# Kernel optimization log

Hardware: AMD Instinct MI355X
Metric: run time of the kernel (lower is better)

The kernel has to match this reference:

```python
import jax, jax.numpy as jnp
import numpy as np

B, S, D, H, L, FFN = 32, 512, 512, 8, 4, 1024
DH = D // H
EPS = 1e-5


def make_pe(seq, d):
    pos = np.arange(seq)[:, None].astype(np.float64)
    i = np.arange(d)[None, :]
    angle = pos / np.power(10000.0, (i // 2 * 2.0) / d)
    pe = angle.copy()
    pe[:, 0::2] = np.sin(angle[:, 0::2])
    pe[:, 1::2] = np.cos(angle[:, 1::2])
    return jnp.asarray(pe, dtype=jnp.float32)


def layer_norm(x, g, b):
    mu = jnp.mean(x, axis=-1, keepdims=True)
    var = jnp.mean((x - mu) ** 2, axis=-1, keepdims=True)
    return (x - mu) * jax.lax.rsqrt(var + EPS) * g + b


def setup_inputs() -> dict:
    key = jax.random.key(0)
    ks = jax.random.split(key, 12)
    sd = 0.02
    d = {
        "x": jax.random.normal(ks[0], (B, S, D), dtype=jnp.float32),
        "pe": make_pe(S, D),
        "Wq": jax.random.normal(ks[1], (L, D, D), dtype=jnp.float32) * sd,
        "bq": jnp.zeros((L, D), dtype=jnp.float32),
        "Wk": jax.random.normal(ks[2], (L, D, D), dtype=jnp.float32) * sd,
        "bk": jnp.zeros((L, D), dtype=jnp.float32),
        "Wv": jax.random.normal(ks[3], (L, D, D), dtype=jnp.float32) * sd,
        "bv": jnp.zeros((L, D), dtype=jnp.float32),
        "Wo": jax.random.normal(ks[4], (L, D, D), dtype=jnp.float32) * sd,
        "bo": jnp.zeros((L, D), dtype=jnp.float32),
        "ln1_g": jnp.ones((L, D), dtype=jnp.float32),
        "ln1_b": jnp.zeros((L, D), dtype=jnp.float32),
        "W1": jax.random.normal(ks[5], (L, D, FFN), dtype=jnp.float32) * sd,
        "b1": jnp.zeros((L, FFN), dtype=jnp.float32),
        "W2": jax.random.normal(ks[6], (L, FFN, D), dtype=jnp.float32) * sd,
        "b2": jnp.zeros((L, D), dtype=jnp.float32),
        "ln2_g": jnp.ones((L, D), dtype=jnp.float32),
        "ln2_b": jnp.zeros((L, D), dtype=jnp.float32),
    }
    return d


def reference(x, pe, Wq, bq, Wk, bk, Wv, bv, Wo, bo, ln1_g, ln1_b,
              W1, b1, W2, b2, ln2_g, ln2_b):
    out = x + pe  # positional encoding (dropout = identity in eval)
    scale = DH ** (-0.5)
    for l in range(L):
        # projections (B,S,D)
        Q = out @ Wq[l] + bq[l]
        K = out @ Wk[l] + bk[l]
        V = out @ Wv[l] + bv[l]
        # faithful raw view (no head transpose), matching torch .view semantics
        Qh = Q.reshape(B * H, S, DH)
        Kh = K.reshape(B * H, S, DH)
        Vh = V.reshape(B * H, S, DH)
        att = jnp.einsum('bqd,bkd->bqk', Qh, Kh) * scale  # (B*H,S,S)
        att = jax.nn.softmax(att, axis=-1)
        ctx = jnp.einsum('bqk,bkd->bqd', att, Vh).reshape(B, S, D)
        a = layer_norm(ctx @ Wo[l] + bo[l] + out, ln1_g[l], ln1_b[l])
        # position-wise FFN
        h = jax.nn.relu(a @ W1[l] + b1[l])
        out = layer_norm(h @ W2[l] + b2[l] + a, ln2_g[l], ln2_b[l])
    return out.reshape(B, S * D)
```

## Files before the change

### kernel.cpp

```cpp
#include <hip/hip_runtime.h>
#include <stdint.h>

#define NB 32
#define NS 512
#define ND 512
#define NH 8
#define NL 4
#define NF 1024
#define NDH 64
#define NM (NB*NS)
#define WLSTRIDE 2097152
#define CSCALE 0.18033688f

typedef __attribute__((ext_vector_type(8))) short bf16x8;
typedef __attribute__((ext_vector_type(4))) short s16x4;
typedef __attribute__((ext_vector_type(4))) float f32x4;
typedef __attribute__((ext_vector_type(2))) uint32_t u32x2;

#define VM0  asm volatile("s_waitcnt vmcnt(0)" ::: "memory")
#define VM4  asm volatile("s_waitcnt vmcnt(4)" ::: "memory")
#define VM8  asm volatile("s_waitcnt vmcnt(8)" ::: "memory")
#define SCHB __builtin_amdgcn_sched_barrier(0)
#define SB   __builtin_amdgcn_s_barrier()

__device__ __forceinline__ short f2bf(float f) {
    union { float f; uint32_t u; } v; v.f = f;
    uint32_t r = (v.u + 0x7FFFu + ((v.u >> 16) & 1u)) >> 16;
    return (short)r;
}
__device__ __forceinline__ float bf2f(short s) {
    union { uint32_t u; float f; } v; v.u = ((uint32_t)(uint16_t)s) << 16;
    return v.f;
}
__device__ __forceinline__ f32x4 mfma16(bf16x8 a, bf16x8 b, f32x4 c) {
    return __builtin_amdgcn_mfma_f32_16x16x32_bf16(a, b, c, 0, 0, 0);
}
__device__ __forceinline__ void gld16(const void* g, void* l) {
    __builtin_amdgcn_global_load_lds(
        (const __attribute__((address_space(1))) void*)g,
        (__attribute__((address_space(3))) void*)l, 16, 0, 0);
}
__device__ __forceinline__ uint32_t cvtpk(float a, float b) {
    uint32_t w;
    asm("v_cvt_pk_bf16_f32 %0, %1, %2" : "=v"(w) : "v"(a), "v"(b));
    return w;
}
__device__ __forceinline__ void xcd_swz(int& bx, int& by, int gx, int gy) {
    int n = gx * gy;
    int f = by * gx + bx;
    int q = n >> 3;
    int xcd = f & 7, idx = f >> 3;
    int s = xcd * q + idx;
    bx = s % gx; by = s / gx;
}

__global__ __launch_bounds__(256) void convT_k(const float* __restrict__ src,
        short* __restrict__ dst, int K, int N, int woff)
{
    __shared__ float T[64][65];
    int tk = K >> 6, tn = N >> 6;
    int bid = blockIdx.x;
    int l = bid / (tk * tn), rb = bid % (tk * tn);
    int k0 = (rb / tn) << 6, n0 = (rb % tn) << 6;
    const float* s = src + (size_t)l * K * N;
    short* d = dst + (size_t)l * WLSTRIDE + woff;
    int tr = threadIdx.x >> 4, tc = threadIdx.x & 15;
    #pragma unroll
    for (int p = 0; p < 4; p++) {
        int row = p * 16 + tr;
        f32x4 v = *(const f32x4*)(s + (size_t)(k0 + row) * N + n0 + tc * 4);
        #pragma unroll
        for (int j = 0; j < 4; j++) T[row][tc * 4 + j] = v[j];
    }
    __syncthreads();
    #pragma unroll
    for (int p = 0; p < 4; p++) {
        int nrow = p * 16 + tr;
        s16x4 w;
        #pragma unroll
        for (int j = 0; j < 4; j++) w[j] = f2bf(T[tc * 4 + j][nrow]);
        *(s16x4*)(d + (size_t)(n0 + nrow) * K + k0 + tc * 4) = w;
    }
}

__global__ __launch_bounds__(256) void biaspack_k(const float* __restrict__ bq,
        const float* __restrict__ bk, const float* __restrict__ bv, float* __restrict__ out)
{
    int i = blockIdx.x * 256 + threadIdx.x;
    if (i >= NL * 1536) return;
    int l = i / 1536, j = i - l * 1536;
    float v = (j < 512) ? bq[l * 512 + j] * CSCALE
            : (j < 1024) ? bk[l * 512 + j - 512] : bv[l * 512 + j - 1024];
    out[i] = v;
}

__global__ __launch_bounds__(256) void addpe_k(const float* __restrict__ x,
        const float* __restrict__ pe, short* __restrict__ X)
{
    size_t i = ((size_t)blockIdx.x * 256 + threadIdx.x) * 8;
    size_t sd = i % (size_t)(NS * ND);
    f32x4 a0 = *(const f32x4*)(x + i);
    f32x4 a1 = *(const f32x4*)(x + i + 4);
    f32x4 p0 = *(const f32x4*)(pe + sd);
    f32x4 p1 = *(const f32x4*)(pe + sd + 4);
    bf16x8 r;
    #pragma unroll
    for (int j = 0; j < 4; j++) { r[j] = f2bf(a0[j] + p0[j]); r[4 + j] = f2bf(a1[j] + p1[j]); }
    *(bf16x8*)(X + i) = r;
}

template<int EPI>
__global__ __launch_bounds__(256) void gemm_bt(
        const short* __restrict__ A, const short* __restrict__ Bt,
        const float* __restrict__ bias, const short* __restrict__ res,
        void* __restrict__ C0, void* __restrict__ C1, void* __restrict__ C2,
        int M, int N, int K)
{
    __shared__ __align__(16) short Al[16384];
    __shared__ __align__(16) short Bl[16384];
    const int tid = threadIdx.x;
    const int wid = tid >> 6, lane = tid & 63;
    int bx = blockIdx.x, by = blockIdx.y;
    xcd_swz(bx, by, gridDim.x, gridDim.y);
    const int m0 = by * 128, n0 = bx * 128;
    const int wr = wid >> 1, wc = wid & 1;

    f32x4 acc[4][4];
    f32x4 zz = {0.f, 0.f, 0.f, 0.f};
    #pragma unroll
    for (int i = 0; i < 4; i++)
        #pragma unroll
        for (int j = 0; j < 4; j++) acc[i][j] = zz;

    const size_t rk = (size_t)K * 2;
    const char* Ab = (const char*)A + (size_t)m0 * rk;
    const char* Bb = (const char*)Bt + (size_t)n0 * rk;

    int srA[4], scA[4], srB[4], scB[4];
    #pragma unroll
    for (int c = 0; c < 4; c++) {
        int p = c * 4096 + tid * 16;
        int la = p ^ (((p >> 7) & 7) << 4);
        srA[c] = la >> 7;  scA[c] = la & 127;
        int lb = p ^ (((p >> 9) & 7) << 4);
        srB[c] = lb >> 7;  scB[c] = lb & 127;
    }

    auto stage = [&](int dofs, int kt) {
        size_t kb = (size_t)(kt << 6) * 2;
        #pragma unroll
        for (int c = 0; c < 4; c++)
            gld16(Ab + (size_t)srA[c] * rk + kb + scA[c],
                  (char*)Al + dofs + c * 4096 + wid * 1024);
        #pragma unroll
        for (int c = 0; c < 4; c++)
            gld16(Bb + (size_t)srB[c] * rk + kb + scB[c],
                  (char*)Bl + dofs + c * 4096 + wid * 1024);
    };
    auto compute = [&](int dofs) {
        #pragma unroll
        for (int ks = 0; ks < 2; ks++) {
            bf16x8 af[4], bfr[4];
            #pragma unroll
            for (int mf = 0; mf < 4; mf++) {
                int row = wr * 64 + mf * 16 + (lane & 15);
                int off = (row * 128 + ks * 64 + ((lane >> 4) * 16)) ^ ((row & 7) << 4);
                af[mf] = *(const bf16x8*)((const char*)Al + dofs + off);
            }
            #pragma unroll
            for (int nf = 0; nf < 4; nf++) {
                int row = wc * 64 + ((lane & 15) << 2) + nf;
                int off = row * 128
                        + ((ks * 64 + ((lane >> 4) * 16)) ^ (((row >> 2) & 7) << 4));
                bfr[nf] = *(const bf16x8*)((const char*)Bl + dofs + off);
            }
            #pragma unroll
            for (int mf = 0; mf < 4; mf++)
                #pragma unroll
                for (int nf = 0; nf < 4; nf++)
                    acc[mf][nf] = mfma16(af[mf], bfr[nf], acc[mf][nf]);
        }
    };

    const int nt = K >> 6;
    stage(0, 0);
    stage(16384, 1);
    VM8; SCHB; SB;
    for (int t = 0; t < nt; t += 2) {
        compute(0);
        SB;
        if (t + 2 < nt) { stage(0, t + 2); VM8; } else VM0;
        SCHB; SB;
        compute(16384);
        SB;
        if (t + 3 < nt) { stage(16384, t + 3); VM8; } else VM0;
        SCHB; SB;
    }

    int seg = 0;
    void* outp;
    int colbase, ostride;
    if (EPI == 0) {
        seg = n0 >> 9;
        outp = (seg == 0) ? C0 : (seg == 1) ? C1 : C2;
        colbase = n0 & 511; ostride = 512;
    } else {
        outp = C0; colbase = n0; ostride = N;
    }

    const int c0 = wc * 64 + ((lane & 15) << 2);
    f32x4 bi4 = *(const f32x4*)(bias + n0 + c0);
    #pragma unroll
    for (int mf = 0; mf < 4; mf++) {
        #pragma unroll
        for (int r = 0; r < 4; r++) {
            int row = m0 + wr * 64 + mf * 16 + ((lane >> 4) << 2) + r;
            float v[4];
            #pragma unroll
            for (int j = 0; j < 4; j++) {
                if (EPI == 0 && seg == 0) v[j] = fmaf(acc[mf][j][r], CSCALE, bi4[j]);
                else                      v[j] = acc[mf][j][r] + bi4[j];
            }
            if (EPI == 0) {
                u32x2 w; w[0] = cvtpk(v[0], v[1]); w[1] = cvtpk(v[2], v[3]);
                *(u32x2*)((short*)outp + (size_t)row * 512 + colbase + c0) = w;
            } else if (EPI == 1) {
                u32x2 w;
                w[0] = cvtpk(fmaxf(v[0], 0.f), fmaxf(v[1], 0.f));
                w[1] = cvtpk(fmaxf(v[2], 0.f), fmaxf(v[3], 0.f));
                *(u32x2*)((short*)outp + (size_t)row * ostride + colbase + c0) = w;
            } else {
                s16x4 rr = *(const s16x4*)(res + (size_t)row * ostride + colbase + c0);
                f32x4 o4;
                #pragma unroll
                for (int j = 0; j < 4; j++) o4[j] = v[j] + bf2f(rr[j]);
                *(f32x4*)((float*)outp + (size_t)row * ostride + colbase + c0) = o4;
            }
        }
    }
}

__global__ __launch_bounds__(256) void vtrans_k(const short* __restrict__ V,
        short* __restrict__ VT)
{
    __shared__ short T[64][65];
    const int tid = threadIdx.x;
    const int r0 = blockIdx.x * 64, g = blockIdx.y;
    const size_t base = (size_t)g * 32768;
    #pragma unroll
    for (int rep = 0; rep < 2; rep++) {
        int chunk = rep * 256 + tid;
        int sr = chunk >> 3, c8 = (chunk & 7) * 8;
        bf16x8 v = *(const bf16x8*)(V + base + (size_t)(r0 + sr) * 64 + c8);
        #pragma unroll
        for (int j = 0; j < 8; j++) T[sr][c8 + j] = v[j];
    }
    __syncthreads();
    #pragma unroll
    for (int rep = 0; rep < 2; rep++) {
        int chunk = rep * 256 + tid;
        int dh = chunk >> 3, c8 = (chunk & 7) * 8;
        bf16x8 w;
        #pragma unroll
        for (int j = 0; j < 8; j++) w[j] = T[c8 + j][dh];
        *(bf16x8*)(VT + base + (size_t)dh * 512 + r0 + c8) = w;
    }
}

__global__ __launch_bounds__(256) void attn_k(
        const short* __restrict__ Q, const short* __restrict__ Kb,
        const short* __restrict__ VT, short* __restrict__ ctx)
{
    __shared__ __align__(16) short Kl[8192];
    __shared__ __align__(16) short Vl[8192];
    __shared__ __align__(16) short Pl[8192];
    const int tid = threadIdx.x, wid = tid >> 6, lane = tid & 63;
    int bx = blockIdx.x, by = blockIdx.y;
    xcd_swz(bx, by, gridDim.x, gridDim.y);
    const int g = by, q0 = bx * 128;
    const size_t base = (size_t)g * 32768;

    bf16x8 qa[2][2];
    #pragma unroll
    for (int qf = 0; qf < 2; qf++)
        #pragma unroll
        for (int ks = 0; ks < 2; ks++)
            qa[qf][ks] = *(const bf16x8*)(Q + base
                + (size_t)(q0 + wid * 32 + qf * 16 + (lane & 15)) * 64
                + ks * 32 + ((lane >> 4) * 8));

    f32x4 o[2][4];
    float ps[2][4];
    f32x4 zz = {0.f, 0.f, 0.f, 0.f};
    #pragma unroll
    for (int qf = 0; qf < 2; qf++) {
        #pragma unroll
        for (int nf = 0; nf < 4; nf++) o[qf][nf] = zz;
        #pragma unroll
        for (int r = 0; r < 4; r++) ps[qf][r] = 0.f;
    }

    const char* Kbase = (const char*)(Kb + base);
    const char* Vbase = (const char*)(VT + base);

    int ksp[2], srow[2], scol[2];
    #pragma unroll
    for (int c = 0; c < 2; c++) {
        int p = c * 4096 + tid * 16;
        ksp[c] = p ^ (((p >> 9) & 7) << 4);
        srow[c] = ksp[c] >> 7;  scol[c] = ksp[c] & 127;
    }

    auto stage = [&](int dofs, int kt) {
        #pragma unroll
        for (int c = 0; c < 2; c++)
            gld16(Kbase + (size_t)kt * 8192 + ksp[c],
                  (char*)Kl + dofs + c * 4096 + wid * 1024);
        #pragma unroll
        for (int c = 0; c < 2; c++)
            gld16(Vbase + (size_t)srow[c] * 1024 + kt * 128 + scol[c],
                  (char*)Vl + dofs + c * 4096 + wid * 1024);
    };

    auto tile = [&](int dofs) {
        f32x4 sc[2][4];
        #pragma unroll
        for (int qf = 0; qf < 2; qf++)
            #pragma unroll
            for (int nf = 0; nf < 4; nf++) sc[qf][nf] = zz;
        #pragma unroll
        for (int ks = 0; ks < 2; ks++) {
            #pragma unroll
            for (int nf = 0; nf < 4; nf++) {
                int kvr = ((lane & 15) << 2) + nf;
                int bo = kvr * 128
                       + ((ks * 64 + ((lane >> 4) * 16)) ^ (((kvr >> 2) & 7) << 4)) + dofs;
                bf16x8 kf = *(const bf16x8*)((const char*)Kl + bo);
                #pragma unroll
                for (int qf = 0; qf < 2; qf++)
                    sc[qf][nf] = mfma16(qa[qf][ks], kf, sc[qf][nf]);
            }
        }

        #pragma unroll
        for (int qf = 0; qf < 2; qf++) {
            #pragma unroll
            for (int r = 0; r < 4; r++) {
                int qr = wid * 32 + qf * 16 + ((lane >> 4) << 2) + r;
                float e0 = __builtin_amdgcn_exp2f(sc[qf][0][r]);
                float e1 = __builtin_amdgcn_exp2f(sc[qf][1][r]);
                float e2 = __builtin_amdgcn_exp2f(sc[qf][2][r]);
                float e3 = __builtin_amdgcn_exp2f(sc[qf][3][r]);
                ps[qf][r] += (e0 + e1) + (e2 + e3);
                u32x2 w;
                w[0] = cvtpk(e0, e1);
                w[1] = cvtpk(e2, e3);
                int bo = (qr * 128 + (lane & 15) * 8) ^ ((qr & 7) << 4);
                *(u32x2*)((char*)Pl + bo) = w;
            }
        }

        #pragma unroll
        for (int ks = 0; ks < 2; ks++) {
            bf16x8 pa[2];
            #pragma unroll
            for (int qf = 0; qf < 2; qf++) {
                int qrb = wid * 32 + qf * 16 + (lane & 15);
                int bo = (qrb * 128 + ks * 64 + ((lane >> 4) * 16)) ^ ((qrb & 7) << 4);
                pa[qf] = *(const bf16x8*)((const char*)Pl + bo);
            }
            #pragma unroll
            for (int nf = 0; nf < 4; nf++) {
                int dh = ((lane & 15) << 2) + nf;
                int bo2 = dh * 128
                        + ((ks * 64 + ((lane >> 4) * 16)) ^ (((dh >> 2) & 7) << 4)) + dofs;
                bf16x8 vf = *(const bf16x8*)((const char*)Vl + bo2);
                #pragma unroll
                for (int qf = 0; qf < 2; qf++)
                    o[qf][nf] = mfma16(pa[qf], vf, o[qf][nf]);
            }
        }
    };

    stage(0, 0);
    stage(8192, 1);
    VM4; SCHB; SB;
    for (int kt = 0; kt < 8; kt += 2) {
        tile(0);
        SB;
        if (kt + 2 < 8) { stage(0, kt + 2); VM4; } else VM0;
        SCHB; SB;
        tile(8192);
        SB;
        if (kt + 3 < 8) { stage(8192, kt + 3); VM4; } else VM0;
        SCHB; SB;
    }

    #pragma unroll
    for (int qf = 0; qf < 2; qf++) {
        #pragma unroll
        for (int r = 0; r < 4; r++) {
            float s = ps[qf][r];
            s += __shfl_xor(s, 1);
            s += __shfl_xor(s, 2);
            s += __shfl_xor(s, 4);
            s += __shfl_xor(s, 8);
            float inv = 1.f / s;
            int qr = q0 + wid * 32 + qf * 16 + ((lane >> 4) << 2) + r;
            u32x2 w;
            w[0] = cvtpk(o[qf][0][r] * inv, o[qf][1][r] * inv);
            w[1] = cvtpk(o[qf][2][r] * inv, o[qf][3][r] * inv);
            *(u32x2*)(ctx + base + (size_t)qr * 64 + ((lane & 15) << 2)) = w;
        }
    }
}

template<int OUTF32>
__global__ __launch_bounds__(256) void ln_k(
        const float* __restrict__ pre, const float* __restrict__ g,
        const float* __restrict__ b, void* __restrict__ out)
{
    int row = blockIdx.x * 4 + (threadIdx.x >> 6);
    int lane = threadIdx.x & 63;
    const float* x = pre + (size_t)row * ND + lane * 8;
    f32x4 a0 = *(const f32x4*)x;
    f32x4 a1 = *(const f32x4*)(x + 4);
    float s = 0.f, sq = 0.f;
    #pragma unroll
    for (int j = 0; j < 4; j++) { s += a0[j]; sq += a0[j] * a0[j]; s += a1[j]; sq += a1[j] * a1[j]; }
    #pragma unroll
    for (int d = 1; d < 64; d <<= 1) { s += __shfl_xor(s, d); sq += __shfl_xor(sq, d); }
    float mean = s * (1.f / ND);
    float var = sq * (1.f / ND) - mean * mean;
    float rstd = rsqrtf(var + 1e-5f);
    const float* gp = g + lane * 8;
    const float* bp = b + lane * 8;
    if (OUTF32) {
        float* op = (float*)out + (size_t)row * ND + lane * 8;
        f32x4 r0, r1;
        #pragma unroll
        for (int j = 0; j < 4; j++) {
            r0[j] = (a0[j] - mean) * rstd * gp[j] + bp[j];
            r1[j] = (a1[j] - mean) * rstd * gp[4 + j] + bp[4 + j];
        }
        *(f32x4*)op = r0;
        *(f32x4*)(op + 4) = r1;
    } else {
        bf16x8 rr;
        #pragma unroll
        for (int j = 0; j < 4; j++) {
            rr[j]     = f2bf((a0[j] - mean) * rstd * gp[j] + bp[j]);
            rr[4 + j] = f2bf((a1[j] - mean) * rstd * gp[4 + j] + bp[4 + j]);
        }
        *(bf16x8*)((short*)out + (size_t)row * ND + lane * 8) = rr;
    }
}

extern "C" void kernel_launch(void* const* d_in, const int* in_sizes, int n_in,
                              void* d_out, int out_size, void* d_ws, size_t ws_size,
                              hipStream_t stream)
{
    (void)in_sizes; (void)n_in; (void)out_size; (void)ws_size;
    const float* x   = (const float*)d_in[0];
    const float* pe  = (const float*)d_in[1];
    const float* Wq  = (const float*)d_in[2];
    const float* bq  = (const float*)d_in[3];
    const float* Wk  = (const float*)d_in[4];
    const float* bk  = (const float*)d_in[5];
    const float* Wv  = (const float*)d_in[6];
    const float* bv  = (const float*)d_in[7];
    const float* Wo  = (const float*)d_in[8];
    const float* bo  = (const float*)d_in[9];
    const float* g1  = (const float*)d_in[10];
    const float* be1 = (const float*)d_in[11];
    const float* W1  = (const float*)d_in[12];
    const float* b1  = (const float*)d_in[13];
    const float* W2  = (const float*)d_in[14];
    const float* b2  = (const float*)d_in[15];
    const float* g2  = (const float*)d_in[16];
    const float* be2 = (const float*)d_in[17];

    char* ws = (char*)d_ws;
    const size_t MB = 1048576;
    short* WT   = (short*)(ws);
    short* XB   = (short*)(ws + 16 * MB);
    short* QB   = (short*)(ws + 32 * MB);
    short* KB   = (short*)(ws + 48 * MB);
    short* VB   = (short*)(ws + 64 * MB);
    short* VTb  = (short*)(ws + 80 * MB);
    short* CT   = (short*)(ws + 96 * MB);
    float* BQKV = (float*)(ws + 112 * MB);
    short* AB   = QB;
    float* PR   = (float*)KB;
    short* HB   = VTb;

    convT_k<<<dim3(NL*8*8),  256, 0, stream>>>(Wq, WT, ND, ND, 0);
    convT_k<<<dim3(NL*8*8),  256, 0, stream>>>(Wk, WT, ND, ND, 262144);
    convT_k<<<dim3(NL*8*8),  256, 0, stream>>>(Wv, WT, ND, ND, 524288);
    convT_k<<<dim3(NL*8*8),  256, 0, stream>>>(Wo, WT, ND, ND, 786432);
    convT_k<<<dim3(NL*8*16), 256, 0, stream>>>(W1, WT, ND, NF, 1048576);
    convT_k<<<dim3(NL*16*8), 256, 0, stream>>>(W2, WT, NF, ND, 1572864);
    biaspack_k<<<dim3(24), 256, 0, stream>>>(bq, bk, bv, BQKV);

    addpe_k<<<dim3(4096), 256, 0, stream>>>(x, pe, XB);

    for (int l = 0; l < NL; l++) {
        const short* wl = WT + (size_t)l * WLSTRIDE;
        gemm_bt<0><<<dim3(12, 128), 256, 0, stream>>>(XB, wl, BQKV + l*1536, nullptr,
                                                      QB, KB, VB, NM, 1536, ND);
        vtrans_k<<<dim3(8, 256), 256, 0, stream>>>(VB, VTb);
        attn_k<<<dim3(4, 256), 256, 0, stream>>>(QB, KB, VTb, CT);
        gemm_bt<2><<<dim3(4, 128), 256, 0, stream>>>(CT, wl + 786432, bo + l*ND, XB,
                                                     PR, nullptr, nullptr, NM, ND, ND);
        ln_k<0><<<dim3(4096), 256, 0, stream>>>(PR, g1 + l*ND, be1 + l*ND, AB);
        gemm_bt<1><<<dim3(8, 128), 256, 0, stream>>>(AB, wl + 1048576, b1 + l*NF, nullptr,
                                                     HB, nullptr, nullptr, NM, NF, ND);
        gemm_bt<2><<<dim3(4, 128), 256, 0, stream>>>(HB, wl + 1572864, b2 + l*ND, AB,
                                                     PR, nullptr, nullptr, NM, ND, NF);
        if (l < NL - 1)
            ln_k<0><<<dim3(4096), 256, 0, stream>>>(PR, g2 + l*ND, be2 + l*ND, XB);
        else
            ln_k<1><<<dim3(4096), 256, 0, stream>>>(PR, g2 + l*ND, be2 + l*ND, (float*)d_out);
    }
}
```

Baseline: 761.1 us.

## Use 256x256-tile 512-thread GEMM for QKV and FFN1 projections

Adds a gemm_big kernel with 256x256 output tiles, 8 waves and 64KB of LDS per stage pair. The QKV projection and the first FFN GEMM now use it, roughly doubling operand reuse per byte loaded from global memory. The residual-epilogue GEMM is specialised to EPI 2 only, and both kernels precompute per-chunk global pointers to cut address arithmetic. Larger tiles mean fewer blocks (384 and 256) and higher register and LDS pressure, which may lower occupancy and load balance across CUs.

Result: no change. 767.5 us (+0.8%).

```diff
diff --git a/kernel.cpp b/kernel.cpp
--- a/kernel.cpp
+++ b/kernel.cpp
@@ -110,11 +110,133 @@
 }
 
 template<int EPI>
+__global__ __launch_bounds__(512) void gemm_big(
+        const short* __restrict__ A, const short* __restrict__ Bt,
+        const float* __restrict__ bias,
+        void* __restrict__ C0, void* __restrict__ C1, void* __restrict__ C2,
+        int M, int N, int K)
+{
+    __shared__ __align__(16) short Al[32768];
+    __shared__ __align__(16) short Bl[32768];
+    const int tid = threadIdx.x;
+    const int wid = tid >> 6, lane = tid & 63;
+    int bx = blockIdx.x, by = blockIdx.y;
+    xcd_swz(bx, by, gridDim.x, gridDim.y);
+    const int m0 = by * 256, n0 = bx * 256;
+    const int wr = wid >> 2, wc = wid & 3;
+
+    f32x4 acc[8][4];
+    f32x4 zz = {0.f, 0.f, 0.f, 0.f};
+    #pragma unroll
+    for (int i = 0; i < 8; i++)
+        #pragma unroll
+        for (int j = 0; j < 4; j++) acc[i][j] = zz;
+
+    const size_t rk = (size_t)K * 2;
+    const char* Ab = (const char*)A + (size_t)m0 * rk;
+    const char* Bb = (const char*)Bt + (size_t)n0 * rk;
+
+    const char* As[4];
+    const char* Bs[4];
+    #pragma unroll
+    for (int c = 0; c < 4; c++) {
+        int p = c * 8192 + tid * 16;
+        int la = p ^ (((p >> 7) & 7) << 4);
+        As[c] = Ab + (size_t)(la >> 7) * rk + (la & 127);
+        int lb = p ^ (((p >> 9) & 7) << 4);
+        Bs[c] = Bb + (size_t)(lb >> 7) * rk + (lb & 127);
+    }
+
+    auto stage = [&](int dofs, int kt) {
+        size_t kb = (size_t)kt << 7;
+        #pragma unroll
+        for (int c = 0; c < 4; c++)
+            gld16(As[c] + kb, (char*)Al + dofs + c * 8192 + wid * 1024);
+        #pragma unroll
+        for (int c = 0; c < 4; c++)
+            gld16(Bs[c] + kb, (char*)Bl + dofs + c * 8192 + wid * 1024);
+    };
+    auto compute = [&](int dofs) {
+        #pragma unroll
+        for (int ks = 0; ks < 2; ks++) {
+            bf16x8 af[8], bfr[4];
+            #pragma unroll
+            for (int mf = 0; mf < 8; mf++) {
+                int row = wr * 128 + mf * 16 + (lane & 15);
+                int off = (row * 128 + ks * 64 + ((lane >> 4) * 16)) ^ ((row & 7) << 4);
+                af[mf] = *(const bf16x8*)((const char*)Al + dofs + off);
+            }
+            #pragma unroll
+            for (int nf = 0; nf < 4; nf++) {
+                int row = wc * 64 + ((lane & 15) << 2) + nf;
+                int off = row * 128
+                        + ((ks * 64 + ((lane >> 4) * 16)) ^ (((row >> 2) & 7) << 4));
+                bfr[nf] = *(const bf16x8*)((const char*)Bl + dofs + off);
+            }
+            #pragma unroll
+            for (int mf = 0; mf < 8; mf++)
+                #pragma unroll
+                for (int nf = 0; nf < 4; nf++)
+                    acc[mf][nf] = mfma16(af[mf], bfr[nf], acc[mf][nf]);
+        }
+    };
+
+    const int nt = K >> 6;
+    stage(0, 0);
+    stage(32768, 1);
+    VM8; SCHB; SB;
+    for (int t = 0; t < nt; t += 2) {
+        compute(0);
+        SB;
+        if (t + 2 < nt) { stage(0, t + 2); VM8; } else VM0;
+        SCHB; SB;
+        compute(32768);
+        SB;
+        if (t + 3 < nt) { stage(32768, t + 3); VM8; } else VM0;
+        SCHB; SB;
+    }
+
+    int seg = 0;
+    void* outp;
+    int colbase, ostride;
+    if (EPI == 0) {
+        seg = n0 >> 9;
+        outp = (seg == 0) ? C0 : (seg == 1) ? C1 : C2;
+        colbase = n0 & 511; ostride = 512;
+    } else {
+        outp = C0; colbase = n0; ostride = N;
+    }
+
+    const int c0 = wc * 64 + ((lane & 15) << 2);
+    f32x4 bi4 = *(const f32x4*)(bias + n0 + c0);
+    #pragma unroll
+    for (int mf = 0; mf < 8; mf++) {
+        #pragma unroll
+        for (int r = 0; r < 4; r++) {
+            int row = m0 + wr * 128 + mf * 16 + ((lane >> 4) << 2) + r;
+            float v[4];
+            #pragma unroll
+            for (int j = 0; j < 4; j++) {
+                if (EPI == 0 && seg == 0) v[j] = fmaf(acc[mf][j][r], CSCALE, bi4[j]);
+                else                      v[j] = acc[mf][j][r] + bi4[j];
+            }
+            u32x2 w;
+            if (EPI == 1) {
+                w[0] = cvtpk(fmaxf(v[0], 0.f), fmaxf(v[1], 0.f));
+                w[1] = cvtpk(fmaxf(v[2], 0.f), fmaxf(v[3], 0.f));
+            } else {
+                w[0] = cvtpk(v[0], v[1]); w[1] = cvtpk(v[2], v[3]);
+            }
+            *(u32x2*)((short*)outp + (size_t)row * ostride + colbase + c0) = w;
+        }
+    }
+}
+
+template<int EPI>
 __global__ __launch_bounds__(256) void gemm_bt(
         const short* __restrict__ A, const short* __restrict__ Bt,
         const float* __restrict__ bias, const short* __restrict__ res,
-        void* __restrict__ C0, void* __restrict__ C1, void* __restrict__ C2,
-        int M, int N, int K)
+        void* __restrict__ C0, int M, int N, int K)
 {
     __shared__ __align__(16) short Al[16384];
     __shared__ __align__(16) short Bl[16384];
@@ -136,26 +258,25 @@
     const char* Ab = (const char*)A + (size_t)m0 * rk;
     const char* Bb = (const char*)Bt + (size_t)n0 * rk;
 
-    int srA[4], scA[4], srB[4], scB[4];
+    const char* As[4];
+    const char* Bs[4];
     #pragma unroll
     for (int c = 0; c < 4; c++) {
         int p = c * 4096 + tid * 16;
         int la = p ^ (((p >> 7) & 7) << 4);
-        srA[c] = la >> 7;  scA[c] = la & 127;
+        As[c] = Ab + (size_t)(la >> 7) * rk + (la & 127);
         int lb = p ^ (((p >> 9) & 7) << 4);
-        srB[c] = lb >> 7;  scB[c] = lb & 127;
+        Bs[c] = Bb + (size_t)(lb >> 7) * rk + (lb & 127);
     }
 
     auto stage = [&](int dofs, int kt) {
-        size_t kb = (size_t)(kt << 6) * 2;
+        size_t kb = (size_t)kt << 7;
         #pragma unroll
         for (int c = 0; c < 4; c++)
-            gld16(Ab + (size_t)srA[c] * rk + kb + scA[c],
-                  (char*)Al + dofs + c * 4096 + wid * 1024);
+            gld16(As[c] + kb, (char*)Al + dofs + c * 4096 + wid * 1024);
         #pragma unroll
         for (int c = 0; c < 4; c++)
-            gld16(Bb + (size_t)srB[c] * rk + kb + scB[c],
-                  (char*)Bl + dofs + c * 4096 + wid * 1024);
+            gld16(Bs[c] + kb, (char*)Bl + dofs + c * 4096 + wid * 1024);
     };
     auto compute = [&](int dofs) {
         #pragma unroll
@@ -197,17 +318,6 @@
         SCHB; SB;
     }
 
-    int seg = 0;
-    void* outp;
-    int colbase, ostride;
-    if (EPI == 0) {
-        seg = n0 >> 9;
-        outp = (seg == 0) ? C0 : (seg == 1) ? C1 : C2;
-        colbase = n0 & 511; ostride = 512;
-    } else {
-        outp = C0; colbase = n0; ostride = N;
-    }
-
     const int c0 = wc * 64 + ((lane & 15) << 2);
     f32x4 bi4 = *(const f32x4*)(bias + n0 + c0);
     #pragma unroll
@@ -217,25 +327,12 @@
             int row = m0 + wr * 64 + mf * 16 + ((lane >> 4) << 2) + r;
             float v[4];
             #pragma unroll
-            for (int j = 0; j < 4; j++) {
-                if (EPI == 0 && seg == 0) v[j] = fmaf(acc[mf][j][r], CSCALE, bi4[j]);
-                else                      v[j] = acc[mf][j][r] + bi4[j];
-            }
-            if (EPI == 0) {
-                u32x2 w; w[0] = cvtpk(v[0], v[1]); w[1] = cvtpk(v[2], v[3]);
-                *(u32x2*)((short*)outp + (size_t)row * 512 + colbase + c0) = w;
-            } else if (EPI == 1) {
-                u32x2 w;
-                w[0] = cvtpk(fmaxf(v[0], 0.f), fmaxf(v[1], 0.f));
-                w[1] = cvtpk(fmaxf(v[2], 0.f), fmaxf(v[3], 0.f));
-                *(u32x2*)((short*)outp + (size_t)row * ostride + colbase + c0) = w;
-            } else {
-                s16x4 rr = *(const s16x4*)(res + (size_t)row * ostride + colbase + c0);
-                f32x4 o4;
-                #pragma unroll
-                for (int j = 0; j < 4; j++) o4[j] = v[j] + bf2f(rr[j]);
-                *(f32x4*)((float*)outp + (size_t)row * ostride + colbase + c0) = o4;
-            }
+            for (int j = 0; j < 4; j++) v[j] = acc[mf][j][r] + bi4[j];
+            s16x4 rr = *(const s16x4*)(res + (size_t)row * N + n0 + c0);
+            f32x4 o4;
+            #pragma unroll
+            for (int j = 0; j < 4; j++) o4[j] = v[j] + bf2f(rr[j]);
+            *(f32x4*)((float*)C0 + (size_t)row * N + n0 + c0) = o4;
         }
     }
 }
@@ -506,17 +603,17 @@
 
     for (int l = 0; l < NL; l++) {
         const short* wl = WT + (size_t)l * WLSTRIDE;
-        gemm_bt<0><<<dim3(12, 128), 256, 0, stream>>>(XB, wl, BQKV + l*1536, nullptr,
-                                                      QB, KB, VB, NM, 1536, ND);
+        gemm_big<0><<<dim3(6, 64), 512, 0, stream>>>(XB, wl, BQKV + l*1536,
+                                                     QB, KB, VB, NM, 1536, ND);
         vtrans_k<<<dim3(8, 256), 256, 0, stream>>>(VB, VTb);
         attn_k<<<dim3(4, 256), 256, 0, stream>>>(QB, KB, VTb, CT);
         gemm_bt<2><<<dim3(4, 128), 256, 0, stream>>>(CT, wl + 786432, bo + l*ND, XB,
-                                                     PR, nullptr, nullptr, NM, ND, ND);
+                                                     PR, NM, ND, ND);
         ln_k<0><<<dim3(4096), 256, 0, stream>>>(PR, g1 + l*ND, be1 + l*ND, AB);
-        gemm_bt<1><<<dim3(8, 128), 256, 0, stream>>>(AB, wl + 1048576, b1 + l*NF, nullptr,
+        gemm_big<1><<<dim3(4, 64), 512, 0, stream>>>(AB, wl + 1048576, b1 + l*NF,
                                                      HB, nullptr, nullptr, NM, NF, ND);
         gemm_bt<2><<<dim3(4, 128), 256, 0, stream>>>(HB, wl + 1572864, b2 + l*ND, AB,
-                                                     PR, nullptr, nullptr, NM, ND, NF);
+                                                     PR, NM, ND, NF);
         if (l < NL - 1)
             ln_k<0><<<dim3(4096), 256, 0, stream>>>(PR, g2 + l*ND, be2 + l*ND, XB);
         else
```

## Convert GEMM double-buffer to triple-buffered LDS ring with MFMA priority boost

Applied to the files above, without the earlier changes.

Converts the GEMM mainloop from a two-stage double buffer into a three-stage ring of LDS buffers, so two tiles are in flight while one is being computed. Global source addresses are now precomputed as pointers per lane, and s_setprio is raised around the MFMA compute section. The aim is to hide global-load latency better and cut address arithmetic. In exchange, LDS use per block grows from 64KB to 96KB, which may reduce the number of blocks resident per CU.

Result: slower. 966.8 us (+27.0%).

```diff
diff --git a/kernel.cpp b/kernel.cpp
--- a/kernel.cpp
+++ b/kernel.cpp
@@ -17,9 +17,10 @@
 typedef __attribute__((ext_vector_type(4))) float f32x4;
 typedef __attribute__((ext_vector_type(2))) uint32_t u32x2;
 
-#define VM0  asm volatile("s_waitcnt vmcnt(0)" ::: "memory")
-#define VM4  asm volatile("s_waitcnt vmcnt(4)" ::: "memory")
-#define VM8  asm volatile("s_waitcnt vmcnt(8)" ::: "memory")
+#define VM0   asm volatile("s_waitcnt vmcnt(0)" ::: "memory")
+#define VM4   asm volatile("s_waitcnt vmcnt(4)" ::: "memory")
+#define VM8   asm volatile("s_waitcnt vmcnt(8)" ::: "memory")
+#define VM16  asm volatile("s_waitcnt vmcnt(16)" ::: "memory")
 #define SCHB __builtin_amdgcn_sched_barrier(0)
 #define SB   __builtin_amdgcn_s_barrier()
 
@@ -110,14 +111,14 @@
 }
 
 template<int EPI>
-__global__ __launch_bounds__(256) void gemm_bt(
+__global__ __launch_bounds__(256) void gemm_ring(
         const short* __restrict__ A, const short* __restrict__ Bt,
         const float* __restrict__ bias, const short* __restrict__ res,
         void* __restrict__ C0, void* __restrict__ C1, void* __restrict__ C2,
         int M, int N, int K)
 {
-    __shared__ __align__(16) short Al[16384];
-    __shared__ __align__(16) short Bl[16384];
+    __shared__ __align__(16) short Al[24576];
+    __shared__ __align__(16) short Bl[24576];
     const int tid = threadIdx.x;
     const int wid = tid >> 6, lane = tid & 63;
     int bx = blockIdx.x, by = blockIdx.y;
@@ -136,28 +137,28 @@
     const char* Ab = (const char*)A + (size_t)m0 * rk;
     const char* Bb = (const char*)Bt + (size_t)n0 * rk;
 
-    int srA[4], scA[4], srB[4], scB[4];
+    const char* As[4];
+    const char* Bs[4];
     #pragma unroll
     for (int c = 0; c < 4; c++) {
         int p = c * 4096 + tid * 16;
         int la = p ^ (((p >> 7) & 7) << 4);
-        srA[c] = la >> 7;  scA[c] = la & 127;
+        As[c] = Ab + (size_t)(la >> 7) * rk + (la & 127);
         int lb = p ^ (((p >> 9) & 7) << 4);
-        srB[c] = lb >> 7;  scB[c] = lb & 127;
+        Bs[c] = Bb + (size_t)(lb >> 7) * rk + (lb & 127);
     }
 
     auto stage = [&](int dofs, int kt) {
-        size_t kb = (size_t)(kt << 6) * 2;
+        size_t kb = (size_t)kt << 7;
         #pragma unroll
         for (int c = 0; c < 4; c++)
-            gld16(Ab + (size_t)srA[c] * rk + kb + scA[c],
-                  (char*)Al + dofs + c * 4096 + wid * 1024);
+            gld16(As[c] + kb, (char*)Al + dofs + c * 4096 + wid * 1024);
         #pragma unroll
         for (int c = 0; c < 4; c++)
-            gld16(Bb + (size_t)srB[c] * rk + kb + scB[c],
-                  (char*)Bl + dofs + c * 4096 + wid * 1024);
+            gld16(Bs[c] + kb, (char*)Bl + dofs + c * 4096 + wid * 1024);
     };
     auto compute = [&](int dofs) {
+        __builtin_amdgcn_s_setprio(1);
         #pragma unroll
         for (int ks = 0; ks < 2; ks++) {
             bf16x8 af[4], bfr[4];
@@ -180,21 +181,23 @@
                 for (int nf = 0; nf < 4; nf++)
                     acc[mf][nf] = mfma16(af[mf], bfr[nf], acc[mf][nf]);
         }
+        __builtin_amdgcn_s_setprio(0);
     };
 
     const int nt = K >> 6;
     stage(0, 0);
     stage(16384, 1);
-    VM8; SCHB; SB;
-    for (int t = 0; t < nt; t += 2) {
-        compute(0);
+    stage(32768, 2);
+    VM16; SCHB; SB;
+    int dofs = 0;
+    for (int t = 0; t < nt; t++) {
+        compute(dofs);
         SB;
-        if (t + 2 < nt) { stage(0, t + 2); VM8; } else VM0;
+        if (t + 3 < nt) { stage(dofs, t + 3); VM16; }
+        else if (t + 2 < nt) VM8;
+        else VM0;
         SCHB; SB;
-        compute(16384);
-        SB;
-        if (t + 3 < nt) { stage(16384, t + 3); VM8; } else VM0;
-        SCHB; SB;
+        dofs = (dofs == 32768) ? 0 : dofs + 16384;
     }
 
     int seg = 0;
@@ -506,17 +509,17 @@
 
     for (int l = 0; l < NL; l++) {
         const short* wl = WT + (size_t)l * WLSTRIDE;
-        gemm_bt<0><<<dim3(12, 128), 256, 0, stream>>>(XB, wl, BQKV + l*1536, nullptr,
-                                                      QB, KB, VB, NM, 1536, ND);
+        gemm_ring<0><<<dim3(12, 128), 256, 0, stream>>>(XB, wl, BQKV + l*1536, nullptr,
+                                                        QB, KB, VB, NM, 1536, ND);
         vtrans_k<<<dim3(8, 256), 256, 0, stream>>>(VB, VTb);
         attn_k<<<dim3(4, 256), 256, 0, stream>>>(QB, KB, VTb, CT);
-        gemm_bt<2><<<dim3(4, 128), 256, 0, stream>>>(CT, wl + 786432, bo + l*ND, XB,
-                                                     PR, nullptr, nullptr, NM, ND, ND);
+        gemm_ring<2><<<dim3(4, 128), 256, 0, stream>>>(CT, wl + 786432, bo + l*ND, XB,
+                                                       PR, nullptr, nullptr, NM, ND, ND);
         ln_k<0><<<dim3(4096), 256, 0, stream>>>(PR, g1 + l*ND, be1 + l*ND, AB);
-        gemm_bt<1><<<dim3(8, 128), 256, 0, stream>>>(AB, wl + 1048576, b1 + l*NF, nullptr,
-                                                     HB, nullptr, nullptr, NM, NF, ND);
-        gemm_bt<2><<<dim3(4, 128), 256, 0, stream>>>(HB, wl + 1572864, b2 + l*ND, AB,
-                                                     PR, nullptr, nullptr, NM, ND, NF);
+        gemm_ring<1><<<dim3(8, 128), 256, 0, stream>>>(AB, wl + 1048576, b1 + l*NF, nullptr,
+                                                       HB, nullptr, nullptr, NM, NF, ND);
+        gemm_ring<2><<<dim3(4, 128), 256, 0, stream>>>(HB, wl + 1572864, b2 + l*ND, AB,
+                                                       PR, nullptr, nullptr, NM, ND, NF);
         if (l < NL - 1)
             ln_k<0><<<dim3(4096), 256, 0, stream>>>(PR, g2 + l*ND, be2 + l*ND, XB);
         else
```
